# Kernel optimization log

Measured on AMD Instinct MI355X. Metric: run time of the kernel, lower is better.

Reference implementation:

```python
import jax, jax.numpy as jnp
import numpy as np

N_EMBEDDING = 32
HEAD_SIZE = 64
B, T = 8, 4096


def setup_inputs() -> dict:
    key = jax.random.key(0)
    kx, kk, kq, kv = jax.random.split(key, 4)
    x = jax.random.normal(kx, (B, T, N_EMBEDDING), dtype=jnp.float32)
    Wk = jax.random.normal(kk, (N_EMBEDDING, HEAD_SIZE), dtype=jnp.float32) * 0.05
    Wq = jax.random.normal(kq, (N_EMBEDDING, HEAD_SIZE), dtype=jnp.float32) * 0.05
    Wv = jax.random.normal(kv, (N_EMBEDDING, HEAD_SIZE), dtype=jnp.float32) * 0.05
    return {"x": x, "Wk": Wk, "Wq": Wq, "Wv": Wv}


def reference(x, Wk, Wq, Wv):
    # x: [B, T, C]; projections (no bias)
    k = jnp.einsum("btc,cd->btd", x, Wk)  # [B,T,D]
    q = jnp.einsum("btc,cd->btd", x, Wq)
    v = jnp.einsum("btc,cd->btd", x, Wv)
    # raw scores (NOTE: original module applies no 1/sqrt(D) scaling)
    wei = jnp.einsum("bqd,bkd->bqk", q, k)  # [B,T,T]
    t = x.shape[1]
    causal = jnp.tril(jnp.ones((t, t), dtype=bool))
    wei = jnp.where(causal[None, :, :], wei, -jnp.inf)
    wei = jax.nn.softmax(wei, axis=-1)
    out = jnp.einsum("bqk,bkd->bqd", wei, v)  # [B,T,D]
    return out
```

## Files before the change

### kernel.cpp

```cpp
#include <hip/hip_runtime.h>
#include <hip/hip_bf16.h>

constexpr int Bc = 8;
constexpr int Tt = 4096;
constexpr int Dd = 64;

typedef __attribute__((ext_vector_type(8))) short short8;
typedef __attribute__((ext_vector_type(4))) float floatx4;
typedef uint4   __attribute__((may_alias)) uint4_a;
typedef short8  __attribute__((may_alias)) short8_a;
typedef ushort4 __attribute__((may_alias)) ushort4_a;
typedef float4  __attribute__((may_alias)) float4_a;

#define MFMA16(A, B, C) __builtin_amdgcn_mfma_f32_16x16x32_bf16(A, B, C, 0, 0, 0)
constexpr float LOG2E = 1.4426950408889634f;

__device__ __forceinline__ unsigned rnd16(float x) {
    unsigned u; __builtin_memcpy(&u, &x, 4); return u + 0x8000u;
}
__device__ __forceinline__ unsigned pk_bf2(float lo, float hi) {
    return __builtin_amdgcn_perm(rnd16(hi), rnd16(lo), 0x07060302);
}
__device__ __forceinline__ ushort4 pack4(floatx4 d) {
    union { unsigned u[2]; ushort4 v; } r;
    r.u[0] = pk_bf2(d[0], d[1]);
    r.u[1] = pk_bf2(d[2], d[3]);
    return r.v;
}
__device__ __forceinline__ short8 cvt8(float4 a, float4 b) {
    union { unsigned u[4]; short8 s; } r;
    r.u[0] = pk_bf2(a.x, a.y);
    r.u[1] = pk_bf2(a.z, a.w);
    r.u[2] = pk_bf2(b.x, b.y);
    r.u[3] = pk_bf2(b.z, b.w);
    return r.s;
}

__global__ __launch_bounds__(1024, 4) void attn_kernel(
    const float* __restrict__ x,
    const float* __restrict__ Wk, const float* __restrict__ Wq,
    const float* __restrict__ Wv,
    float* __restrict__ out)
{
    __shared__ uint4 sStage[4096];
    __shared__ uint4 sP[2048];
    __shared__ uint4 sG[128];

    int b  = blockIdx.x & 7;
    int pr = blockIdx.x >> 3;
    int tid  = threadIdx.x;
    int wave = tid >> 6, lane = tid & 63;
    int group = wave >> 2, gw = wave & 3;
    int ln15 = lane & 15, quad = lane >> 4;
    size_t bT = (size_t)b * Tt;

    const int tg = tid & 255;
    const int srow = tg >> 2, scg = tg & 3;
    const int skg = srow >> 3, srl = srow & 7;

    if (wave == 0) {
        floatx4 gC[2][2];
        #pragma unroll
        for (int mt = 0; mt < 2; ++mt)
            #pragma unroll
            for (int nt = 0; nt < 2; ++nt) gC[mt][nt] = (floatx4){0.f,0.f,0.f,0.f};
        #pragma unroll
        for (int kt = 0; kt < 2; ++kt) {
            short8 aG[2], bG[2];
            #pragma unroll
            for (int mt = 0; mt < 2; ++mt) {
                const float* qp = Wq + (ln15 + 16*mt)*64 + 32*kt + quad*8;
                float4 a = ((const float4_a*)qp)[0], bb = ((const float4_a*)qp)[1];
                a.x*=LOG2E; a.y*=LOG2E; a.z*=LOG2E; a.w*=LOG2E;
                bb.x*=LOG2E; bb.y*=LOG2E; bb.z*=LOG2E; bb.w*=LOG2E;
                aG[mt] = cvt8(a, bb);
                const float* kp = Wk + (ln15 + 16*mt)*64 + 32*kt + quad*8;
                bG[mt] = cvt8(((const float4_a*)kp)[0], ((const float4_a*)kp)[1]);
            }
            #pragma unroll
            for (int mt = 0; mt < 2; ++mt)
                #pragma unroll
                for (int nt = 0; nt < 2; ++nt)
                    gC[mt][nt] = MFMA16(aG[mt], bG[nt], gC[mt][nt]);
        }
        unsigned short* sGh = (unsigned short*)sG;
        #pragma unroll
        for (int mt = 0; mt < 2; ++mt)
            #pragma unroll
            for (int nt = 0; nt < 2; ++nt)
                *(ushort4_a*)(sGh + (16*nt + ln15)*32 + 16*mt + quad*4)
                    = pack4(gC[mt][nt]);
    }
    __syncthreads();

    const int gBase = group * 1024;
    unsigned short* sYh = (unsigned short*)sP;

    for (int phase = 0; phase < 2; ++phase) {
        const int qtP = phase ? pr : 63 - pr;
        const int q0 = qtP * 64;
        const int qrow = q0 + gw*16 + ln15;

        float4 pX0, pX1;
        if (group <= qtP) {
            const float* xp = x + (bT + group*64 + srow)*32 + scg*8;
            pX0 = ((const float4_a*)xp)[0];
            pX1 = ((const float4_a*)xp)[1];
        }

        if (wave < 8) {
            int qs = wave & 3, mt = wave >> 2;
            union { uint4 u; short8 s; } g;
            g.u = sG[(16*mt + ln15)*4 + quad];
            const float* xp = x + (bT + q0 + qs*16 + ln15)*32 + quad*8;
            short8 xq = cvt8(((const float4_a*)xp)[0], ((const float4_a*)xp)[1]);
            floatx4 d = (floatx4){0.f,0.f,0.f,0.f};
            d = MFMA16(g.s, xq, d);
            *(ushort4_a*)(sYh + (qs*16 + ln15)*32 + 16*mt + quad*4) = pack4(d);
        }
        __syncthreads();
        short8 bq;
        {
            union { uint4 u; short8 s; } t0;
            t0.u = sP[(gw*16 + ln15)*4 + quad];
            bq = t0.s;
        }

        floatx4 z4[2];
        z4[0] = (floatx4){0.f,0.f,0.f,0.f};
        z4[1] = (floatx4){0.f,0.f,0.f,0.f};
        float l_lane = 0.f;

        const int nIter = (qtP + 4) >> 2;

        for (int it = 0; it < nIter; ++it) {
            int kt = 4*it + group;
            bool active = (kt <= qtP);
            const int stB = gBase + (it & 1) * 512;
            if (active) {
                unsigned u0 = pk_bf2(pX0.x, pX0.y), u1 = pk_bf2(pX0.z, pX0.w);
                unsigned u2 = pk_bf2(pX1.x, pX1.y), u3 = pk_bf2(pX1.z, pX1.w);
                uint4 xu; xu.x = u0; xu.y = u1; xu.z = u2; xu.w = u3;
                sStage[stB + srow*4 + (scg ^ (srow & 3))] = xu;
                unsigned short* sXh = (unsigned short*)(sStage + stB + 256);
                int cb = scg * 8;
                sXh[(cb+0)*64 + ((skg ^ 0) << 3) + srl] = (unsigned short)(u0 & 0xffff);
                sXh[(cb+1)*64 + ((skg ^ 1) << 3) + srl] = (unsigned short)(u0 >> 16);
                sXh[(cb+2)*64 + ((skg ^ 2) << 3) + srl] = (unsigned short)(u1 & 0xffff);
                sXh[(cb+3)*64 + ((skg ^ 3) << 3) + srl] = (unsigned short)(u1 >> 16);
                sXh[(cb+4)*64 + ((skg ^ 4) << 3) + srl] = (unsigned short)(u2 & 0xffff);
                sXh[(cb+5)*64 + ((skg ^ 5) << 3) + srl] = (unsigned short)(u2 >> 16);
                sXh[(cb+6)*64 + ((skg ^ 6) << 3) + srl] = (unsigned short)(u3 & 0xffff);
                sXh[(cb+7)*64 + ((skg ^ 7) << 3) + srl] = (unsigned short)(u3 >> 16);
            }
            __syncthreads();
            int ktn = kt + 4;
            if (ktn <= qtP) {
                const float* xp = x + (bT + ktn*64 + srow)*32 + scg*8;
                pX0 = ((const float4_a*)xp)[0];
                pX1 = ((const float4_a*)xp)[1];
            }
            if (!active) continue;
            int k0 = kt * 64;

            const int xsw = quad ^ (ln15 & 3);
            floatx4 s4[4];
            #pragma unroll
            for (int t = 0; t < 4; ++t) {
                union { uint4 u; short8 s; } a;
                a.u = sStage[stB + (16*t + ln15)*4 + xsw];
                floatx4 c = (floatx4){0.f,0.f,0.f,0.f};
                c = MFMA16(a.s, bq, c);
                s4[t] = c;
            }

            unsigned long long* sP64 = (unsigned long long*)sP;
            const int pb = wave*256 + ln15*16;
            const int xk = ln15 & 14;
            if (kt == qtP) {
                #pragma unroll
                for (int t = 0; t < 4; ++t) {
                    int keyb = k0 + 16*t + quad*4;
                    float p[4];
                    #pragma unroll
                    for (int r = 0; r < 4; ++r) {
                        p[r] = (keyb + r <= qrow) ? __builtin_amdgcn_exp2f(s4[t][r]) : 0.f;
                        l_lane += p[r];
                    }
                    unsigned long long pk =
                        ((unsigned long long)pk_bf2(p[2], p[3]) << 32) | pk_bf2(p[0], p[1]);
                    sP64[pb + ((4*t + quad) ^ xk)] = pk;
                }
            } else {
                #pragma unroll
                for (int t = 0; t < 4; ++t) {
                    float p[4];
                    #pragma unroll
                    for (int r = 0; r < 4; ++r) {
                        p[r] = __builtin_amdgcn_exp2f(s4[t][r]);
                        l_lane += p[r];
                    }
                    unsigned long long pk =
                        ((unsigned long long)pk_bf2(p[2], p[3]) << 32) | pk_bf2(p[0], p[1]);
                    sP64[pb + ((4*t + quad) ^ xk)] = pk;
                }
            }

            int h = (ln15 >> 1) & 7;
            union { uint4 u; short8 s; } p0, p1;
            p0.u = sP[wave*128 + ln15*8 + (quad ^ h)];
            p1.u = sP[wave*128 + ln15*8 + ((quad + 4) ^ h)];
            const int h7 = ln15 & 7;
            #pragma unroll
            for (int mt = 0; mt < 2; ++mt) {
                int row = 16*mt + ln15;
                union { uint4 u; short8 s; } a0, a1;
                a0.u = sStage[stB + 256 + row*8 + (quad ^ h7)];
                a1.u = sStage[stB + 256 + row*8 + ((quad + 4) ^ h7)];
                z4[mt] = MFMA16(a0.s, p0.s, z4[mt]);
                z4[mt] = MFMA16(a1.s, p1.s, z4[mt]);
            }
        }

        __syncthreads();
        int li = gw*64 + lane;
        ((float*)sP)[wave*64 + lane] = l_lane;
        if (group != 0) {
            float4* st = (float4*)(sStage + group*1024);
            st[li*2 + 0] = make_float4(z4[0][0], z4[0][1], z4[0][2], z4[0][3]);
            st[li*2 + 1] = make_float4(z4[1][0], z4[1][1], z4[1][2], z4[1][3]);
        }
        __syncthreads();
        if (group == 0) {
            short8 wv_f[4];
            #pragma unroll
            for (int t = 0; t < 4; ++t) {
                int col = 16*t + ln15;
                union { unsigned u[4]; short8 s; } rv;
                #pragma unroll
                for (int jj = 0; jj < 4; ++jj) {
                    const float* v0 = Wv + (quad*8 + 2*jj) * 64 + col;
                    rv.u[jj] = pk_bf2(v0[0], v0[64]);
                }
                wv_f[t] = rv.s;
            }
            float l = l_lane + ((float*)sP)[256 + li]
                    + ((float*)sP)[512 + li] + ((float*)sP)[768 + li];
            l += __shfl_xor(l, 16);
            l += __shfl_xor(l, 32);
            float inv = 1.f / l;
            #pragma unroll
            for (int g = 1; g < 4; ++g) {
                float4* st = (float4*)(sStage + g*1024);
                float4 a = st[li*2 + 0], bb = st[li*2 + 1];
                z4[0][0]+=a.x; z4[0][1]+=a.y; z4[0][2]+=a.z; z4[0][3]+=a.w;
                z4[1][0]+=bb.x; z4[1][1]+=bb.y; z4[1][2]+=bb.z; z4[1][3]+=bb.w;
            }
            unsigned short* sZb = (unsigned short*)sStage;
            #pragma unroll
            for (int mt = 0; mt < 2; ++mt)
                *(ushort4_a*)(sZb + (gw*16 + ln15)*32 + 16*mt + quad*4) = pack4(z4[mt]);
            union { uint4 u; short8 s; } zb;
            zb.u = sStage[(gw*16 + ln15)*4 + quad];
            #pragma unroll
            for (int t = 0; t < 4; ++t) {
                floatx4 o = (floatx4){0.f,0.f,0.f,0.f};
                o = MFMA16(wv_f[t], zb.s, o);
                *(float4_a*)(out + (bT + q0 + gw*16 + ln15)*Dd + 16*t + quad*4)
                    = make_float4(o[0]*inv, o[1]*inv, o[2]*inv, o[3]*inv);
            }
        }
        __syncthreads();
    }
}

extern "C" void kernel_launch(void* const* d_in, const int* in_sizes, int n_in,
                              void* d_out, int out_size, void* d_ws, size_t ws_size,
                              hipStream_t stream)
{
    const float* x  = (const float*)d_in[0];
    const float* Wk = (const float*)d_in[1];
    const float* Wq = (const float*)d_in[2];
    const float* Wv = (const float*)d_in[3];
    float* out = (float*)d_out;

    attn_kernel<<<Bc * 32, 1024, 0, stream>>>(x, Wk, Wq, Wv, out);
}
```

Measured before the change: 90.28 us.

## Feed P directly from registers via fp16 MFMA, dropping P shared-memory round trip

Switches the P·X accumulation from bf16 16x16x32 MFMA to fp16 16x16x16 MFMA so the softmax probabilities, already in the accumulator layout, can be packed straight into B operands without going through shared memory. The transposed X tile is now stored as fp16 with a new swizzle matching the 4-element operand layout, and the P shared buffer shrinks accordingly. This removes LDS writes/reads and a layout shuffle per key tile, at the cost of twice as many (smaller) MFMA instructions and fp16 rounding via round-toward-zero conversion.

New measurement: 86.95 us, median of 2. 3.7% less time.

```diff
diff --git a/kernel.cpp b/kernel.cpp
--- a/kernel.cpp
+++ b/kernel.cpp
@@ -7,12 +7,16 @@
 
 typedef __attribute__((ext_vector_type(8))) short short8;
 typedef __attribute__((ext_vector_type(4))) float floatx4;
+typedef __attribute__((ext_vector_type(4))) __fp16 half4;
+typedef __attribute__((ext_vector_type(2))) __fp16 half2v;
 typedef uint4   __attribute__((may_alias)) uint4_a;
 typedef short8  __attribute__((may_alias)) short8_a;
 typedef ushort4 __attribute__((may_alias)) ushort4_a;
 typedef float4  __attribute__((may_alias)) float4_a;
-
-#define MFMA16(A, B, C) __builtin_amdgcn_mfma_f32_16x16x32_bf16(A, B, C, 0, 0, 0)
+typedef half4   __attribute__((may_alias)) half4_a;
+
+#define MFMA16(A, B, C)  __builtin_amdgcn_mfma_f32_16x16x32_bf16(A, B, C, 0, 0, 0)
+#define MFMAH16(A, B, C) __builtin_amdgcn_mfma_f32_16x16x16f16(A, B, C, 0, 0, 0)
 constexpr float LOG2E = 1.4426950408889634f;
 
 __device__ __forceinline__ unsigned rnd16(float x) {
@@ -43,7 +47,7 @@
     float* __restrict__ out)
 {
     __shared__ uint4 sStage[4096];
-    __shared__ uint4 sP[2048];
+    __shared__ uint4 sP[256];
     __shared__ uint4 sG[128];
 
     int b  = blockIdx.x & 7;
@@ -56,7 +60,6 @@
 
     const int tg = tid & 255;
     const int srow = tg >> 2, scg = tg & 3;
-    const int skg = srow >> 3, srl = srow & 7;
 
     if (wave == 0) {
         floatx4 gC[2][2];
@@ -142,16 +145,20 @@
                 unsigned u2 = pk_bf2(pX1.x, pX1.y), u3 = pk_bf2(pX1.z, pX1.w);
                 uint4 xu; xu.x = u0; xu.y = u1; xu.z = u2; xu.w = u3;
                 sStage[stB + srow*4 + (scg ^ (srow & 3))] = xu;
+                union { half2v h; unsigned short us[2]; } w01, w23, w45, w67;
+                w01.h = __builtin_amdgcn_cvt_pkrtz(pX0.x, pX0.y);
+                w23.h = __builtin_amdgcn_cvt_pkrtz(pX0.z, pX0.w);
+                w45.h = __builtin_amdgcn_cvt_pkrtz(pX1.x, pX1.y);
+                w67.h = __builtin_amdgcn_cvt_pkrtz(pX1.z, pX1.w);
+                unsigned short hv[8] = { w01.us[0], w01.us[1], w23.us[0], w23.us[1],
+                                         w45.us[0], w45.us[1], w67.us[0], w67.us[1] };
                 unsigned short* sXh = (unsigned short*)(sStage + stB + 256);
-                int cb = scg * 8;
-                sXh[(cb+0)*64 + ((skg ^ 0) << 3) + srl] = (unsigned short)(u0 & 0xffff);
-                sXh[(cb+1)*64 + ((skg ^ 1) << 3) + srl] = (unsigned short)(u0 >> 16);
-                sXh[(cb+2)*64 + ((skg ^ 2) << 3) + srl] = (unsigned short)(u1 & 0xffff);
-                sXh[(cb+3)*64 + ((skg ^ 3) << 3) + srl] = (unsigned short)(u1 >> 16);
-                sXh[(cb+4)*64 + ((skg ^ 4) << 3) + srl] = (unsigned short)(u2 & 0xffff);
-                sXh[(cb+5)*64 + ((skg ^ 5) << 3) + srl] = (unsigned short)(u2 >> 16);
-                sXh[(cb+6)*64 + ((skg ^ 6) << 3) + srl] = (unsigned short)(u3 & 0xffff);
-                sXh[(cb+7)*64 + ((skg ^ 7) << 3) + srl] = (unsigned short)(u3 >> 16);
+                const int cb = scg * 8, gx = srow >> 2, ko = srow & 3;
+                #pragma unroll
+                for (int jj = 0; jj < 8; ++jj) {
+                    int c = cb + jj;
+                    sXh[c*64 + ((gx ^ (c & 15)) << 2) + ko] = hv[jj];
+                }
             }
             __syncthreads();
             int ktn = kt + 4;
@@ -174,51 +181,40 @@
                 s4[t] = c;
             }
 
-            unsigned long long* sP64 = (unsigned long long*)sP;
-            const int pb = wave*256 + ln15*16;
-            const int xk = ln15 & 14;
             if (kt == qtP) {
                 #pragma unroll
                 for (int t = 0; t < 4; ++t) {
                     int keyb = k0 + 16*t + quad*4;
-                    float p[4];
                     #pragma unroll
                     for (int r = 0; r < 4; ++r) {
-                        p[r] = (keyb + r <= qrow) ? __builtin_amdgcn_exp2f(s4[t][r]) : 0.f;
-                        l_lane += p[r];
+                        float p = (keyb + r <= qrow) ? __builtin_amdgcn_exp2f(s4[t][r]) : 0.f;
+                        s4[t][r] = p;
+                        l_lane += p;
                     }
-                    unsigned long long pk =
-                        ((unsigned long long)pk_bf2(p[2], p[3]) << 32) | pk_bf2(p[0], p[1]);
-                    sP64[pb + ((4*t + quad) ^ xk)] = pk;
                 }
             } else {
                 #pragma unroll
-                for (int t = 0; t < 4; ++t) {
-                    float p[4];
+                for (int t = 0; t < 4; ++t)
                     #pragma unroll
                     for (int r = 0; r < 4; ++r) {
-                        p[r] = __builtin_amdgcn_exp2f(s4[t][r]);
-                        l_lane += p[r];
+                        float p = __builtin_amdgcn_exp2f(s4[t][r]);
+                        s4[t][r] = p;
+                        l_lane += p;
                     }
-                    unsigned long long pk =
-                        ((unsigned long long)pk_bf2(p[2], p[3]) << 32) | pk_bf2(p[0], p[1]);
-                    sP64[pb + ((4*t + quad) ^ xk)] = pk;
-                }
-            }
-
-            int h = (ln15 >> 1) & 7;
-            union { uint4 u; short8 s; } p0, p1;
-            p0.u = sP[wave*128 + ln15*8 + (quad ^ h)];
-            p1.u = sP[wave*128 + ln15*8 + ((quad + 4) ^ h)];
-            const int h7 = ln15 & 7;
-            #pragma unroll
-            for (int mt = 0; mt < 2; ++mt) {
-                int row = 16*mt + ln15;
-                union { uint4 u; short8 s; } a0, a1;
-                a0.u = sStage[stB + 256 + row*8 + (quad ^ h7)];
-                a1.u = sStage[stB + 256 + row*8 + ((quad + 4) ^ h7)];
-                z4[mt] = MFMA16(a0.s, p0.s, z4[mt]);
-                z4[mt] = MFMA16(a1.s, p1.s, z4[mt]);
+            }
+
+            const unsigned short* sXh = (const unsigned short*)(sStage + stB + 256);
+            #pragma unroll
+            for (int t = 0; t < 4; ++t) {
+                union { half2v h2[2]; half4 h4; } pb;
+                pb.h2[0] = __builtin_amdgcn_cvt_pkrtz(s4[t][0], s4[t][1]);
+                pb.h2[1] = __builtin_amdgcn_cvt_pkrtz(s4[t][2], s4[t][3]);
+                const int gph = ((4*t + quad) ^ ln15) << 2;
+                #pragma unroll
+                for (int mt = 0; mt < 2; ++mt) {
+                    half4 xa = *(const half4_a*)(sXh + (16*mt + ln15)*64 + gph);
+                    z4[mt] = MFMAH16(xa, pb.h4, z4[mt]);
+                }
             }
         }
 
```
